# Kernel tuning notes

Hardware: AMD Instinct MI355X
Metric: run time of the kernel (lower is better)

Reference implementation:

```python
import jax, jax.numpy as jnp
import numpy as np

B, S, M, D, H = 16, 128, 128, 256, 256  # batch, src nodes, max neighbors, emb dim, hidden dim


def setup_inputs() -> dict:
    key = jax.random.key(0)
    k1, k2, k3, k4 = jax.random.split(key, 4)
    src = jax.random.normal(k1, (B, S, M, D), dtype=jnp.float32)
    neigh = jax.random.normal(k2, (B, S, M, D), dtype=jnp.float32)
    # ragged neighbor lists: zero out rows past each node's neighbor count,
    # matching the torch module's all-zero-row padding convention
    lens = jax.random.randint(k3, (B, S), 1, M + 1)
    valid = (jnp.arange(M)[None, None, :] < lens[:, :, None]).astype(jnp.float32)
    neigh = neigh * valid[..., None]
    W_map = jax.random.normal(k4, (2 * D, H), dtype=jnp.float32) * np.float32(1.0 / np.sqrt(2 * D))
    b_map = jnp.zeros((H,), dtype=jnp.float32)
    return {"src_node_features": src, "neigh_node_features": neigh, "W_map": W_map, "b_map": b_map}


def reference(src_node_features, neigh_node_features, W_map, b_map):
    # NeighborAggregator, method='mean': count non-all-zero neighbor rows, masked mean
    valid = jnp.any(neigh_node_features != 0, axis=-1)            # [B, S, M]
    num = jnp.sum(valid, axis=-1).astype(src_node_features.dtype)  # [B, S]
    neigh_mean = neigh_node_features.sum(axis=2) / jnp.maximum(num, 1.0)[..., None]  # [B, S, D]
    # SynGCNLayer, agg_hidden_method='concat'
    hidden = jnp.concatenate([src_node_features.sum(axis=2), neigh_mean], axis=-1)  # [B, S, 2D]
    # filter_nonsource_nodes: all src slots populated -> identity reshape to [B*S, 2D]
    hidden = hidden.reshape(-1, hidden.shape[-1])
    out = jax.nn.leaky_relu(hidden @ W_map + b_map, negative_slope=0.01)  # [B*S, H]
    # normalize=False, dropout is identity in eval
    return out
```

## Files before the change

### kernel.cpp

```cpp
#include <hip/hip_runtime.h>

#define Bdim 16
#define Sdim 128
#define Mdim 128
#define Ddim 256
#define Hdim 256

__global__ __launch_bounds__(256) void gcn_fused_kernel(
    const float* __restrict__ src,
    const float* __restrict__ neigh,
    const float* __restrict__ Wmap,
    const float* __restrict__ bmap,
    float* __restrict__ out)
{
    const int node = blockIdx.x;
    const int tid  = threadIdx.x;
    const int wave = tid >> 6;
    const int lane = tid & 63;

    const size_t base = (size_t)node * (Mdim * Ddim);
    const float4* __restrict__ src4 = (const float4*)(src + base);
    const float4* __restrict__ ngh4 = (const float4*)(neigh + base);

    float4 sacc = make_float4(0.f, 0.f, 0.f, 0.f);
    float4 nacc = make_float4(0.f, 0.f, 0.f, 0.f);
    int cnt = 0;

    #pragma unroll 4
    for (int m = wave; m < Mdim; m += 4) {
        const int idx = m * (Ddim / 4) + lane;
        float4 sv = src4[idx];
        float4 nv = ngh4[idx];
        sacc.x += sv.x; sacc.y += sv.y; sacc.z += sv.z; sacc.w += sv.w;
        nacc.x += nv.x; nacc.y += nv.y; nacc.z += nv.z; nacc.w += nv.w;
        int nz = (nv.x != 0.f) || (nv.y != 0.f) || (nv.z != 0.f) || (nv.w != 0.f);
        if (__any(nz)) cnt++;
    }

    __shared__ float s_s[4][Ddim];
    __shared__ float s_n[4][Ddim];
    __shared__ int   s_cnt[4];
    __shared__ float hidden[2 * Ddim];

    const int dbase = lane * 4;
    s_s[wave][dbase + 0] = sacc.x;
    s_s[wave][dbase + 1] = sacc.y;
    s_s[wave][dbase + 2] = sacc.z;
    s_s[wave][dbase + 3] = sacc.w;
    s_n[wave][dbase + 0] = nacc.x;
    s_n[wave][dbase + 1] = nacc.y;
    s_n[wave][dbase + 2] = nacc.z;
    s_n[wave][dbase + 3] = nacc.w;
    if (lane == 0) s_cnt[wave] = cnt;
    __syncthreads();

    const float num = (float)(s_cnt[0] + s_cnt[1] + s_cnt[2] + s_cnt[3]);
    const float inv = 1.0f / fmaxf(num, 1.0f);

    const float ssum = s_s[0][tid] + s_s[1][tid] + s_s[2][tid] + s_s[3][tid];
    const float nsum = s_n[0][tid] + s_n[1][tid] + s_n[2][tid] + s_n[3][tid];
    hidden[tid]        = ssum;
    hidden[Ddim + tid] = nsum * inv;
    __syncthreads();

    float acc = bmap[tid];
    const float4* __restrict__ h4 = (const float4*)hidden;
    #pragma unroll 4
    for (int k4 = 0; k4 < (2 * Ddim) / 4; ++k4) {
        const float4 h = h4[k4];
        const int k = k4 * 4;
        acc += h.x * Wmap[(size_t)(k + 0) * Hdim + tid];
        acc += h.y * Wmap[(size_t)(k + 1) * Hdim + tid];
        acc += h.z * Wmap[(size_t)(k + 2) * Hdim + tid];
        acc += h.w * Wmap[(size_t)(k + 3) * Hdim + tid];
    }
    const float r = acc > 0.f ? acc : 0.01f * acc;
    out[(size_t)node * Hdim + tid] = r;
}

extern "C" void kernel_launch(void* const* d_in, const int* in_sizes, int n_in,
                              void* d_out, int out_size, void* d_ws, size_t ws_size,
                              hipStream_t stream) {
    const float* src   = (const float*)d_in[0];
    const float* neigh = (const float*)d_in[1];
    const float* Wmap  = (const float*)d_in[2];
    const float* bmap  = (const float*)d_in[3];
    float* out = (float*)d_out;

    dim3 grid(Bdim * Sdim);
    dim3 block(256);
    gcn_fused_kernel<<<grid, block, 0, stream>>>(src, neigh, Wmap, bmap, out);
}
```

Measured before the change: 542.4 us.

## Process four nodes per block with batched loads and shared weight reads

Each 512-thread block now handles four nodes. Two waves per node split the neighbor rows, and each thread issues four float4 loads from both inputs before accumulating, which raises memory-level parallelism. In the projection, each thread computes two output rows that share every W_map load, halving weight traffic per node. Shared memory grows and the grid shrinks to a quarter, which could reduce scheduling flexibility. The main cost stays the streaming read of two large inputs.

```diff
diff --git a/kernel.cpp b/kernel.cpp
--- a/kernel.cpp
+++ b/kernel.cpp
@@ -5,77 +5,101 @@
 #define Mdim 128
 #define Ddim 256
 #define Hdim 256
+#define NPB 4
+#define NT  512
 
-__global__ __launch_bounds__(256) void gcn_fused_kernel(
+__global__ __launch_bounds__(NT, 4) void gcn_fused2(
     const float* __restrict__ src,
     const float* __restrict__ neigh,
     const float* __restrict__ Wmap,
     const float* __restrict__ bmap,
     float* __restrict__ out)
 {
-    const int node = blockIdx.x;
-    const int tid  = threadIdx.x;
-    const int wave = tid >> 6;
-    const int lane = tid & 63;
+    const int tid   = threadIdx.x;
+    const int wave  = tid >> 6;
+    const int lane  = tid & 63;
+    const int lnode = wave >> 1;
+    const int mph   = wave & 1;
 
-    const size_t base = (size_t)node * (Mdim * Ddim);
-    const float4* __restrict__ src4 = (const float4*)(src + base);
-    const float4* __restrict__ ngh4 = (const float4*)(neigh + base);
+    const size_t base4 = (size_t)(blockIdx.x * NPB + lnode) * (Mdim * Ddim / 4);
+    const float4* __restrict__ src4 = (const float4*)src + base4;
+    const float4* __restrict__ ngh4 = (const float4*)neigh + base4;
 
     float4 sacc = make_float4(0.f, 0.f, 0.f, 0.f);
     float4 nacc = make_float4(0.f, 0.f, 0.f, 0.f);
     int cnt = 0;
 
-    #pragma unroll 4
-    for (int m = wave; m < Mdim; m += 4) {
-        const int idx = m * (Ddim / 4) + lane;
-        float4 sv = src4[idx];
-        float4 nv = ngh4[idx];
-        sacc.x += sv.x; sacc.y += sv.y; sacc.z += sv.z; sacc.w += sv.w;
-        nacc.x += nv.x; nacc.y += nv.y; nacc.z += nv.z; nacc.w += nv.w;
-        int nz = (nv.x != 0.f) || (nv.y != 0.f) || (nv.z != 0.f) || (nv.w != 0.f);
-        if (__any(nz)) cnt++;
+    for (int i0 = 0; i0 < 64; i0 += 4) {
+        float4 sv[4], nv[4];
+        #pragma unroll
+        for (int j = 0; j < 4; ++j) {
+            const int m   = mph + 2 * (i0 + j);
+            const int idx = m * (Ddim / 4) + lane;
+            sv[j] = src4[idx];
+            nv[j] = ngh4[idx];
+        }
+        #pragma unroll
+        for (int j = 0; j < 4; ++j) {
+            sacc.x += sv[j].x; sacc.y += sv[j].y; sacc.z += sv[j].z; sacc.w += sv[j].w;
+            nacc.x += nv[j].x; nacc.y += nv[j].y; nacc.z += nv[j].z; nacc.w += nv[j].w;
+            int nz = (nv[j].x != 0.f) | (nv[j].y != 0.f) | (nv[j].z != 0.f) | (nv[j].w != 0.f);
+            if (__any(nz)) cnt++;
+        }
     }
 
-    __shared__ float s_s[4][Ddim];
-    __shared__ float s_n[4][Ddim];
-    __shared__ int   s_cnt[4];
-    __shared__ float hidden[2 * Ddim];
+    __shared__ float s_s[8][Ddim];
+    __shared__ float s_n[8][Ddim];
+    __shared__ int   s_cnt[8];
+    __shared__ float hid[NPB][2 * Ddim];
 
-    const int dbase = lane * 4;
-    s_s[wave][dbase + 0] = sacc.x;
-    s_s[wave][dbase + 1] = sacc.y;
-    s_s[wave][dbase + 2] = sacc.z;
-    s_s[wave][dbase + 3] = sacc.w;
-    s_n[wave][dbase + 0] = nacc.x;
-    s_n[wave][dbase + 1] = nacc.y;
-    s_n[wave][dbase + 2] = nacc.z;
-    s_n[wave][dbase + 3] = nacc.w;
+    *(float4*)&s_s[wave][lane * 4] = sacc;
+    *(float4*)&s_n[wave][lane * 4] = nacc;
     if (lane == 0) s_cnt[wave] = cnt;
     __syncthreads();
 
-    const float num = (float)(s_cnt[0] + s_cnt[1] + s_cnt[2] + s_cnt[3]);
-    const float inv = 1.0f / fmaxf(num, 1.0f);
-
-    const float ssum = s_s[0][tid] + s_s[1][tid] + s_s[2][tid] + s_s[3][tid];
-    const float nsum = s_n[0][tid] + s_n[1][tid] + s_n[2][tid] + s_n[3][tid];
-    hidden[tid]        = ssum;
-    hidden[Ddim + tid] = nsum * inv;
+    {
+        const int t    = tid & (Ddim - 1);
+        const int half = tid >> 8;
+        #pragma unroll
+        for (int n = 0; n < NPB; ++n) {
+            if (half == 0) {
+                hid[n][t] = s_s[2 * n][t] + s_s[2 * n + 1][t];
+            } else {
+                const float num = (float)(s_cnt[2 * n] + s_cnt[2 * n + 1]);
+                const float inv = 1.0f / fmaxf(num, 1.0f);
+                hid[n][Ddim + t] = (s_n[2 * n][t] + s_n[2 * n + 1][t]) * inv;
+            }
+        }
+    }
     __syncthreads();
 
-    float acc = bmap[tid];
-    const float4* __restrict__ h4 = (const float4*)hidden;
+    const int t  = tid & (Ddim - 1);
+    const int n0 = (tid >> 8) * 2;
+    float acc0 = bmap[t];
+    float acc1 = acc0;
+    const float4* __restrict__ h0 = (const float4*)hid[n0];
+    const float4* __restrict__ h1 = (const float4*)hid[n0 + 1];
+
     #pragma unroll 4
     for (int k4 = 0; k4 < (2 * Ddim) / 4; ++k4) {
-        const float4 h = h4[k4];
+        const float4 ha = h0[k4];
+        const float4 hb = h1[k4];
         const int k = k4 * 4;
-        acc += h.x * Wmap[(size_t)(k + 0) * Hdim + tid];
-        acc += h.y * Wmap[(size_t)(k + 1) * Hdim + tid];
-        acc += h.z * Wmap[(size_t)(k + 2) * Hdim + tid];
-        acc += h.w * Wmap[(size_t)(k + 3) * Hdim + tid];
+        const float w0 = Wmap[(size_t)(k + 0) * Hdim + t];
+        const float w1 = Wmap[(size_t)(k + 1) * Hdim + t];
+        const float w2 = Wmap[(size_t)(k + 2) * Hdim + t];
+        const float w3 = Wmap[(size_t)(k + 3) * Hdim + t];
+        acc0 = fmaf(ha.x, w0, acc0); acc1 = fmaf(hb.x, w0, acc1);
+        acc0 = fmaf(ha.y, w1, acc0); acc1 = fmaf(hb.y, w1, acc1);
+        acc0 = fmaf(ha.z, w2, acc0); acc1 = fmaf(hb.z, w2, acc1);
+        acc0 = fmaf(ha.w, w3, acc0); acc1 = fmaf(hb.w, w3, acc1);
     }
-    const float r = acc > 0.f ? acc : 0.01f * acc;
-    out[(size_t)node * Hdim + tid] = r;
+
+    const float r0 = acc0 > 0.f ? acc0 : 0.01f * acc0;
+    const float r1 = acc1 > 0.f ? acc1 : 0.01f * acc1;
+    const size_t row0 = (size_t)blockIdx.x * NPB + n0;
+    out[row0 * Hdim + t]       = r0;
+    out[(row0 + 1) * Hdim + t] = r1;
 }
 
 extern "C" void kernel_launch(void* const* d_in, const int* in_sizes, int n_in,
@@ -87,7 +111,7 @@
     const float* bmap  = (const float*)d_in[3];
     float* out = (float*)d_out;
 
-    dim3 grid(Bdim * Sdim);
-    dim3 block(256);
-    gcn_fused_kernel<<<grid, block, 0, stream>>>(src, neigh, Wmap, bmap, out);
+    dim3 grid((Bdim * Sdim) / NPB);
+    dim3 block(NT);
+    gcn_fused2<<<grid, block, 0, stream>>>(src, neigh, Wmap, bmap, out);
 }
```

Result: faster. 519.4 us (-4.3%).

## Split fused kernel into batched-load reduction and multi-row GEMV kernels

Applied to the files above, without the earlier changes.

Splits the per-node fused kernel into a persistent reduction kernel and a separate GEMM kernel that shares a workspace buffer. The reduction issues eight independent float4 loads per tensor before accumulating, to raise memory-level parallelism on the bandwidth-bound input stream. The GEMM computes four output rows per thread so each weight load is reused, cutting repeated W reads. It adds a second launch and a round trip of the hidden matrix through global memory.

```diff
diff --git a/kernel.cpp b/kernel.cpp
--- a/kernel.cpp
+++ b/kernel.cpp
@@ -5,77 +5,108 @@
 #define Mdim 128
 #define Ddim 256
 #define Hdim 256
+#define NNODE (Bdim * Sdim)
+#define KK (2 * Ddim)
 
-__global__ __launch_bounds__(256) void gcn_fused_kernel(
+#define A_GRID 512
+#define A_NPB (NNODE / A_GRID)
+
+__global__ __launch_bounds__(256, 2) void gcn_reduce(
     const float* __restrict__ src,
     const float* __restrict__ neigh,
+    float* __restrict__ hidden)
+{
+    const int tid  = threadIdx.x;
+    const int wave = tid >> 6;
+    const int lane = tid & 63;
+
+    __shared__ float s_s[4][Ddim];
+    __shared__ float s_n[4][Ddim];
+    __shared__ int   s_cnt[4];
+
+    for (int ln = 0; ln < A_NPB; ++ln) {
+        const int node = blockIdx.x * A_NPB + ln;
+        const float4* __restrict__ src4 =
+            (const float4*)src + (size_t)node * (Mdim * Ddim / 4);
+        const float4* __restrict__ ngh4 =
+            (const float4*)neigh + (size_t)node * (Mdim * Ddim / 4);
+
+        float4 sacc = make_float4(0.f, 0.f, 0.f, 0.f);
+        float4 nacc = make_float4(0.f, 0.f, 0.f, 0.f);
+        int cnt = 0;
+
+        for (int b = wave; b < 16; b += 4) {
+            const int m0 = b * 8;
+            float4 sv[8], nv[8];
+            #pragma unroll
+            for (int j = 0; j < 8; ++j)
+                sv[j] = src4[(m0 + j) * (Ddim / 4) + lane];
+            #pragma unroll
+            for (int j = 0; j < 8; ++j)
+                nv[j] = ngh4[(m0 + j) * (Ddim / 4) + lane];
+            #pragma unroll
+            for (int j = 0; j < 8; ++j) {
+                sacc.x += sv[j].x; sacc.y += sv[j].y;
+                sacc.z += sv[j].z; sacc.w += sv[j].w;
+                nacc.x += nv[j].x; nacc.y += nv[j].y;
+                nacc.z += nv[j].z; nacc.w += nv[j].w;
+                int nz = (nv[j].x != 0.f) | (nv[j].y != 0.f) |
+                         (nv[j].z != 0.f) | (nv[j].w != 0.f);
+                if (__any(nz)) cnt++;
+            }
+        }
+
+        *(float4*)&s_s[wave][lane * 4] = sacc;
+        *(float4*)&s_n[wave][lane * 4] = nacc;
+        if (lane == 0) s_cnt[wave] = cnt;
+        __syncthreads();
+
+        {
+            const float num = (float)(s_cnt[0] + s_cnt[1] + s_cnt[2] + s_cnt[3]);
+            const float inv = 1.0f / fmaxf(num, 1.0f);
+            const float ss = s_s[0][tid] + s_s[1][tid] + s_s[2][tid] + s_s[3][tid];
+            const float ns = s_n[0][tid] + s_n[1][tid] + s_n[2][tid] + s_n[3][tid];
+            hidden[(size_t)node * KK + tid]        = ss;
+            hidden[(size_t)node * KK + Ddim + tid] = ns * inv;
+        }
+        __syncthreads();
+    }
+}
+
+#define B_GRID 256
+
+__global__ __launch_bounds__(512, 2) void gcn_gemm(
+    const float* __restrict__ hidden,
     const float* __restrict__ Wmap,
     const float* __restrict__ bmap,
     float* __restrict__ out)
 {
-    const int node = blockIdx.x;
-    const int tid  = threadIdx.x;
-    const int wave = tid >> 6;
-    const int lane = tid & 63;
+    const int t    = threadIdx.x & (Hdim - 1);
+    const int half = threadIdx.x >> 8;
+    const int r0   = blockIdx.x * 8 + half * 4;
 
-    const size_t base = (size_t)node * (Mdim * Ddim);
-    const float4* __restrict__ src4 = (const float4*)(src + base);
-    const float4* __restrict__ ngh4 = (const float4*)(neigh + base);
+    const float* __restrict__ h = hidden + (size_t)r0 * KK;
 
-    float4 sacc = make_float4(0.f, 0.f, 0.f, 0.f);
-    float4 nacc = make_float4(0.f, 0.f, 0.f, 0.f);
-    int cnt = 0;
+    const float bv = bmap[t];
+    float acc0 = bv, acc1 = bv, acc2 = bv, acc3 = bv;
 
-    #pragma unroll 4
-    for (int m = wave; m < Mdim; m += 4) {
-        const int idx = m * (Ddim / 4) + lane;
-        float4 sv = src4[idx];
-        float4 nv = ngh4[idx];
-        sacc.x += sv.x; sacc.y += sv.y; sacc.z += sv.z; sacc.w += sv.w;
-        nacc.x += nv.x; nacc.y += nv.y; nacc.z += nv.z; nacc.w += nv.w;
-        int nz = (nv.x != 0.f) || (nv.y != 0.f) || (nv.z != 0.f) || (nv.w != 0.f);
-        if (__any(nz)) cnt++;
+    #pragma unroll 8
+    for (int k = 0; k < KK; ++k) {
+        const float wv = Wmap[(size_t)k * Hdim + t];
+        acc0 = fmaf(h[k],          wv, acc0);
+        acc1 = fmaf(h[KK + k],     wv, acc1);
+        acc2 = fmaf(h[2 * KK + k], wv, acc2);
+        acc3 = fmaf(h[3 * KK + k], wv, acc3);
     }
 
-    __shared__ float s_s[4][Ddim];
-    __shared__ float s_n[4][Ddim];
-    __shared__ int   s_cnt[4];
-    __shared__ float hidden[2 * Ddim];
-
-    const int dbase = lane * 4;
-    s_s[wave][dbase + 0] = sacc.x;
-    s_s[wave][dbase + 1] = sacc.y;
-    s_s[wave][dbase + 2] = sacc.z;
-    s_s[wave][dbase + 3] = sacc.w;
-    s_n[wave][dbase + 0] = nacc.x;
-    s_n[wave][dbase + 1] = nacc.y;
-    s_n[wave][dbase + 2] = nacc.z;
-    s_n[wave][dbase + 3] = nacc.w;
-    if (lane == 0) s_cnt[wave] = cnt;
-    __syncthreads();
-
-    const float num = (float)(s_cnt[0] + s_cnt[1] + s_cnt[2] + s_cnt[3]);
-    const float inv = 1.0f / fmaxf(num, 1.0f);
-
-    const float ssum = s_s[0][tid] + s_s[1][tid] + s_s[2][tid] + s_s[3][tid];
-    const float nsum = s_n[0][tid] + s_n[1][tid] + s_n[2][tid] + s_n[3][tid];
-    hidden[tid]        = ssum;
-    hidden[Ddim + tid] = nsum * inv;
-    __syncthreads();
-
-    float acc = bmap[tid];
-    const float4* __restrict__ h4 = (const float4*)hidden;
-    #pragma unroll 4
-    for (int k4 = 0; k4 < (2 * Ddim) / 4; ++k4) {
-        const float4 h = h4[k4];
-        const int k = k4 * 4;
-        acc += h.x * Wmap[(size_t)(k + 0) * Hdim + tid];
-        acc += h.y * Wmap[(size_t)(k + 1) * Hdim + tid];
-        acc += h.z * Wmap[(size_t)(k + 2) * Hdim + tid];
-        acc += h.w * Wmap[(size_t)(k + 3) * Hdim + tid];
-    }
-    const float r = acc > 0.f ? acc : 0.01f * acc;
-    out[(size_t)node * Hdim + tid] = r;
+    const float r0v = acc0 > 0.f ? acc0 : 0.01f * acc0;
+    const float r1v = acc1 > 0.f ? acc1 : 0.01f * acc1;
+    const float r2v = acc2 > 0.f ? acc2 : 0.01f * acc2;
+    const float r3v = acc3 > 0.f ? acc3 : 0.01f * acc3;
+    out[(size_t)(r0 + 0) * Hdim + t] = r0v;
+    out[(size_t)(r0 + 1) * Hdim + t] = r1v;
+    out[(size_t)(r0 + 2) * Hdim + t] = r2v;
+    out[(size_t)(r0 + 3) * Hdim + t] = r3v;
 }
 
 extern "C" void kernel_launch(void* const* d_in, const int* in_sizes, int n_in,
@@ -85,9 +116,9 @@
     const float* neigh = (const float*)d_in[1];
     const float* Wmap  = (const float*)d_in[2];
     const float* bmap  = (const float*)d_in[3];
-    float* out = (float*)d_out;
+    float* out    = (float*)d_out;
+    float* hidden = (float*)d_ws;
 
-    dim3 grid(Bdim * Sdim);
-    dim3 block(256);
-    gcn_fused_kernel<<<grid, block, 0, stream>>>(src, neigh, Wmap, bmap, out);
+    gcn_reduce<<<dim3(A_GRID), dim3(256), 0, stream>>>(src, neigh, hidden);
+    gcn_gemm<<<dim3(B_GRID), dim3(512), 0, stream>>>(hidden, Wmap, bmap, out);
 }
```

New measurement: 553.2 us. Within noise of the previous version (+2.0%).
